# Optimization experiments

Hardware: AMD Instinct MI355X
Metric: run time of the kernel (lower is better)

The kernel has to match this reference:

```python
import jax, jax.numpy as jnp
import numpy as np

B, N, C, H = 2, 4096, 256, 4
DH = C // H  # 64
EPS = 1e-6
TEMPERATURE = 1.0


def setup_inputs() -> dict:
    key = jax.random.key(0)
    ks = jax.random.split(key, 12)
    s = 0.02
    return {
        "x": jax.random.normal(ks[0], (B, N, C), dtype=jnp.float32),
        "pos_embed": jax.random.normal(ks[1], (B, N, C), dtype=jnp.float32),
        # per-head Q/K/V linear weights stacked over heads (torch Linear(dim, dim_head))
        "Wq": jax.random.normal(ks[2], (H, C, DH), dtype=jnp.float32) * s,
        "bq": jax.random.normal(ks[3], (H, DH), dtype=jnp.float32) * s,
        "Wk": jax.random.normal(ks[4], (H, C, DH), dtype=jnp.float32) * s,
        "bk": jax.random.normal(ks[5], (H, DH), dtype=jnp.float32) * s,
        "Wv": jax.random.normal(ks[6], (H, C, DH), dtype=jnp.float32) * s,
        "bv": jax.random.normal(ks[7], (H, DH), dtype=jnp.float32) * s,
        "Wo": jax.random.normal(ks[8], (C, C), dtype=jnp.float32) * s,
        "bo": jax.random.normal(ks[9], (C,), dtype=jnp.float32) * s,
        "ln_g": jnp.ones((C,), dtype=jnp.float32),
        "ln_b": jnp.zeros((C,), dtype=jnp.float32),
    }


def reference(x, pos_embed, Wq, bq, Wk, bk, Wv, bv, Wo, bo, ln_g, ln_b):
    dk = TEMPERATURE * jnp.sqrt(jnp.float32(DH))
    # pre-norm: x + pos_embed -> dropout(p=0, identity) -> LayerNorm(eps=1e-6)
    h = x + pos_embed
    mu = jnp.mean(h, axis=-1, keepdims=True)
    var = jnp.mean(jnp.square(h - mu), axis=-1, keepdims=True)
    h = (h - mu) * jax.lax.rsqrt(var + EPS) * ln_g + ln_b  # [B,N,C]
    # all heads at once (original loops over heads with separate small Linears)
    q = jnp.einsum("bnc,hcd->bhnd", h, Wq) + bq[None, :, None, :]
    k = jnp.einsum("bnc,hcd->bhnd", h, Wk) + bk[None, :, None, :]
    v = jnp.einsum("bnc,hcd->bhnd", h, Wv) + bv[None, :, None, :]
    scores = jnp.einsum("bhid,bhjd->bhij", q, k) / dk  # [B,H,N,N]
    # NOTE: original uses F.softmax(dot_prod, dim=1) on [B,N,N] -> normalize over
    # the QUERY axis i, not the key axis j. Replicated faithfully here (axis=2).
    attn = jax.nn.softmax(scores, axis=2)
    o = jnp.einsum("bhij,bhjd->bhid", attn, v)  # [B,H,N,DH]
    o = jnp.transpose(o, (0, 2, 1, 3)).reshape(B, N, C)  # concat heads on channel
    return o @ Wo + bo
```

## Files before the change

kernel.cpp:

```cpp
#include <hip/hip_runtime.h>
#include <math.h>

#define B_ 2
#define N_ 4096
#define C_ 256
#define H_ 4
#define DH_ 64
#define EPS_ 1e-6f
#define SCALE_Q_ 0.18033688011112042f

typedef short bf16x8 __attribute__((ext_vector_type(8)));
typedef float f32x4 __attribute__((ext_vector_type(4)));
typedef int i32x4 __attribute__((ext_vector_type(4)));

#define MFMA32(a, b, c) __builtin_amdgcn_mfma_f32_16x16x32_bf16(a, b, c, 0, 0, 0)
#define FAST_EXP2(x) __builtin_amdgcn_exp2f(x)

__device__ __forceinline__ unsigned short f2bf(float x) {
  unsigned int u = __float_as_uint(x);
  return (unsigned short)((u + 0x7FFFu + ((u >> 16) & 1u)) >> 16);
}
__device__ __forceinline__ float bf2f(unsigned short u) {
  return __uint_as_float(((unsigned int)u) << 16);
}
__device__ __forceinline__ int pack2bf(float lo, float hi) {
  return (int)__builtin_amdgcn_perm(__float_as_uint(hi) + 0x8000u,
                                    __float_as_uint(lo) + 0x8000u, 0x07060302u);
}

__global__ __launch_bounds__(256) void ln_kernel(
    const float* __restrict__ x, const float* __restrict__ pos,
    const float* __restrict__ g, const float* __restrict__ beta,
    unsigned short* __restrict__ h16) {
  const int row = blockIdx.x;
  const int t = threadIdx.x;
  const int w = t >> 6;
  float val = x[row * C_ + t] + pos[row * C_ + t];
  __shared__ float sm[8];
  float s = val;
  s += __shfl_xor(s, 1);  s += __shfl_xor(s, 2);  s += __shfl_xor(s, 4);
  s += __shfl_xor(s, 8);  s += __shfl_xor(s, 16); s += __shfl_xor(s, 32);
  if ((t & 63) == 0) sm[w] = s;
  __syncthreads();
  const float mu = (sm[0] + sm[1] + sm[2] + sm[3]) * (1.0f / C_);
  const float d = val - mu;
  float v = d * d;
  v += __shfl_xor(v, 1);  v += __shfl_xor(v, 2);  v += __shfl_xor(v, 4);
  v += __shfl_xor(v, 8);  v += __shfl_xor(v, 16); v += __shfl_xor(v, 32);
  if ((t & 63) == 0) sm[4 + w] = v;
  __syncthreads();
  const float var = (sm[4] + sm[5] + sm[6] + sm[7]) * (1.0f / C_);
  h16[row * C_ + t] = f2bf(d * rsqrtf(var + EPS_) * g[t] + beta[t]);
}

__global__ __launch_bounds__(256) void wconv_kernel(
    const float* __restrict__ Wq, const float* __restrict__ Wk,
    const float* __restrict__ Wv, const float* __restrict__ Wo,
    unsigned short* __restrict__ W3T, unsigned short* __restrict__ WoT) {
  const int base = blockIdx.x * 2048;
#pragma unroll
  for (int p = 0; p < 8; p++) {
    const int idx = base + p * 256 + threadIdx.x;
    if (idx < 196608) {
      const int m = idx >> 14;
      const int rem = idx & 16383;
      const int c = rem >> 6, d = rem & 63;
      const int h = m / 3, kind = m - h * 3;
      const float* W = kind == 0 ? Wq : kind == 1 ? Wk : Wv;
      float v = W[h * 16384 + rem];
      if (kind == 0) v *= SCALE_Q_;
      W3T[(h * 192 + kind * 64 + d) * 256 + c] = f2bf(v);
    } else {
      const int widx = idx - 196608;
      const int k = widx >> 8, n = widx & 255;
      WoT[n * 256 + k] = f2bf(Wo[widx]);
    }
  }
}

__global__ __launch_bounds__(256) void qkv_kernel(
    const unsigned short* __restrict__ h16, const unsigned short* __restrict__ W3T,
    const float* __restrict__ bq, const float* __restrict__ bk,
    const float* __restrict__ bv,
    unsigned short* __restrict__ q16, unsigned short* __restrict__ k16,
    unsigned short* __restrict__ vT16) {
  const int rt = blockIdx.x;
  const int hh = blockIdx.y;
  const int t = threadIdx.x;
  const int w = t >> 6, lane = t & 63, c = lane & 15, quad = lane >> 4;
  __shared__ unsigned short Hs[128 * 64];
  __shared__ unsigned short Bs[192 * 64];
  const int row0 = rt * 128;

  f32x4 acc[2][12];
#pragma unroll
  for (int mi = 0; mi < 2; mi++)
#pragma unroll
    for (int nt = 0; nt < 12; nt++) acc[mi][nt] = (f32x4){0.f, 0.f, 0.f, 0.f};

  for (int kt = 0; kt < C_; kt += 64) {
    __syncthreads();
#pragma unroll
    for (int p = 0; p < 4; p++) {
      const int e = t + p * 256;
      const int row = e >> 3, ch = e & 7;
      *(bf16x8*)&Hs[row * 64 + ((ch ^ (row & 7)) * 8)] =
          *(const bf16x8*)&h16[(size_t)(row0 + row) * C_ + kt + ch * 8];
    }
#pragma unroll
    for (int p = 0; p < 6; p++) {
      const int e = t + p * 256;
      const int row = e >> 3, ch = e & 7;
      *(bf16x8*)&Bs[row * 64 + ((ch ^ (row & 7)) * 8)] =
          *(const bf16x8*)&W3T[(size_t)(hh * 192 + row) * C_ + kt + ch * 8];
    }
    __syncthreads();
#pragma unroll
    for (int kh = 0; kh < 2; kh++) {
      bf16x8 a[2];
#pragma unroll
      for (int mi = 0; mi < 2; mi++) {
        const int i = w * 32 + mi * 16 + c;
        a[mi] = *(const bf16x8*)&Hs[i * 64 + (((kh * 4 + quad) ^ (i & 7)) * 8)];
      }
#pragma unroll
      for (int nt = 0; nt < 12; nt++) {
        const int n = nt * 16 + c;
        bf16x8 b = *(const bf16x8*)&Bs[n * 64 + (((kh * 4 + quad) ^ (n & 7)) * 8)];
        acc[0][nt] = MFMA32(a[0], b, acc[0][nt]);
        acc[1][nt] = MFMA32(a[1], b, acc[1][nt]);
      }
    }
  }
#pragma unroll
  for (int nt = 0; nt < 12; nt++) {
    const int kind = nt >> 2;
    const int col = (nt & 3) * 16 + c;
    const float bias = kind == 0 ? bq[hh * 64 + col] * SCALE_Q_
                     : kind == 1 ? bk[hh * 64 + col] : bv[hh * 64 + col];
#pragma unroll
    for (int mi = 0; mi < 2; mi++) {
#pragma unroll
      for (int r = 0; r < 4; r++) {
        const int gr = row0 + w * 32 + mi * 16 + quad * 4 + r;
        const int b = gr >> 12, n = gr & (N_ - 1);
        const size_t bh = (size_t)(b * H_ + hh);
        const unsigned short val = f2bf(acc[mi][nt][r] + bias);
        if (kind == 0)      q16[(bh * N_ + n) * DH_ + col] = val;
        else if (kind == 1) k16[(bh * N_ + n) * DH_ + col] = val;
        else                vT16[(bh * DH_ + col) * N_ + n] = val;
      }
    }
  }
}

__global__ __launch_bounds__(256, 2) void colstats_kernel(
    const unsigned short* __restrict__ q16, const unsigned short* __restrict__ k16,
    unsigned short* __restrict__ vT16) {
  const int blk = blockIdx.x;
  const int bh = blk & 7;
  const int j0 = (blk >> 3) * 64;
  const int t = threadIdx.x;
  const int w = t >> 6, lane = t & 63, c = lane & 15, quad = lane >> 4;
  __shared__ unsigned short Qs[64 * 64];
  __shared__ float Lp[4][64];
  __shared__ float ilv[64];

  bf16x8 ka[4][2];
#pragma unroll
  for (int jb = 0; jb < 4; jb++) {
    const size_t kb = ((size_t)bh * N_ + j0 + jb * 16 + c) * DH_;
    ka[jb][0] = *(const bf16x8*)&k16[kb + quad * 8];
    ka[jb][1] = *(const bf16x8*)&k16[kb + 32 + quad * 8];
  }

  bf16x8 pre[2];
  auto loadQ = [&](int i0) {
#pragma unroll
    for (int p = 0; p < 2; p++) {
      const int e = t + p * 256;
      const int row = e >> 3, ch = e & 7;
      pre[p] = *(const bf16x8*)&q16[((size_t)bh * N_ + i0 + row) * DH_ + ch * 8];
    }
  };
  loadQ(0);

  f32x4 lsum[4];
#pragma unroll
  for (int jb = 0; jb < 4; jb++) lsum[jb] = (f32x4){0.f, 0.f, 0.f, 0.f};

  for (int i0 = 0; i0 < N_; i0 += 64) {
    __syncthreads();
#pragma unroll
    for (int p = 0; p < 2; p++) {
      const int e = t + p * 256;
      const int row = e >> 3, ch = e & 7;
      *(bf16x8*)&Qs[row * 64 + ((ch ^ (row & 7)) * 8)] = pre[p];
    }
    __syncthreads();
    if (i0 + 64 < N_) loadQ(i0 + 64);
    const int ir = w * 16 + c;
    bf16x8 qf0 = *(const bf16x8*)&Qs[ir * 64 + ((quad ^ (c & 7)) * 8)];
    bf16x8 qf1 = *(const bf16x8*)&Qs[ir * 64 + (((4 + quad) ^ (c & 7)) * 8)];
#pragma unroll
    for (int jb = 0; jb < 4; jb++) {
      f32x4 s = {0.f, 0.f, 0.f, 0.f};
      s = MFMA32(ka[jb][0], qf0, s);
      s = MFMA32(ka[jb][1], qf1, s);
#pragma unroll
      for (int r = 0; r < 4; r++) lsum[jb][r] += FAST_EXP2(s[r]);
    }
  }
#pragma unroll
  for (int jb = 0; jb < 4; jb++) {
#pragma unroll
    for (int r = 0; r < 4; r++) {
      float s = lsum[jb][r];
      s += __shfl_xor(s, 1); s += __shfl_xor(s, 2);
      s += __shfl_xor(s, 4); s += __shfl_xor(s, 8);
      if (c == 0) Lp[w][jb * 16 + quad * 4 + r] = s;
    }
  }
  __syncthreads();
  if (t < 64) ilv[t] = 1.0f / (Lp[0][t] + Lp[1][t] + Lp[2][t] + Lp[3][t]);
  __syncthreads();
#pragma unroll
  for (int p = 0; p < 2; p++) {
    const int e = t + p * 256;
    const int d = e >> 3, ch = e & 7;
    const size_t addr = ((size_t)bh * DH_ + d) * N_ + j0 + ch * 8;
    bf16x8 v = *(const bf16x8*)&vT16[addr];
#pragma unroll
    for (int jj = 0; jj < 8; jj++)
      v[jj] = (short)f2bf(bf2f((unsigned short)v[jj]) * ilv[ch * 8 + jj]);
    *(bf16x8*)&vT16[addr] = v;
  }
}

__global__ __launch_bounds__(256, 2) void attnout_kernel(
    const unsigned short* __restrict__ q16, const unsigned short* __restrict__ k16,
    const unsigned short* __restrict__ vT16, unsigned short* __restrict__ ob16) {
  const int blk = blockIdx.x;
  const int bh = blk & 7;
  const int bb = bh >> 2, hh = bh & 3;
  const int i0 = (blk >> 3) * 64;
  const int t = threadIdx.x;
  const int w = t >> 6, lane = t & 63, c = lane & 15, quad = lane >> 4;

  __shared__ unsigned short Ks[128 * 64];
  __shared__ unsigned short Vs[64 * 128];
  __shared__ float Rbuf[4096];

  bf16x8 qa[4][2];
#pragma unroll
  for (int ib = 0; ib < 4; ib++) {
    const size_t qb = ((size_t)bh * N_ + i0 + ib * 16 + c) * DH_;
    qa[ib][0] = *(const bf16x8*)&q16[qb + quad * 8];
    qa[ib][1] = *(const bf16x8*)&q16[qb + 32 + quad * 8];
  }

  bf16x8 kpre[4], vpre[4];
  auto loadKV = [&](int jt) {
#pragma unroll
    for (int p = 0; p < 4; p++) {
      const int e = t + p * 256;
      kpre[p] = *(const bf16x8*)&k16[((size_t)bh * N_ + jt + (e >> 3)) * DH_ + (e & 7) * 8];
      vpre[p] = *(const bf16x8*)&vT16[((size_t)bh * DH_ + (e >> 4)) * N_ + jt + (e & 15) * 8];
    }
  };
  loadKV(0);

  f32x4 of[4][4];
#pragma unroll
  for (int ib = 0; ib < 4; ib++)
#pragma unroll
    for (int dt = 0; dt < 4; dt++) of[ib][dt] = (f32x4){0.f, 0.f, 0.f, 0.f};

  const int jw = w * 32;
  for (int jt = 0; jt < N_; jt += 128) {
    __syncthreads();
#pragma unroll
    for (int p = 0; p < 4; p++) {
      const int e = t + p * 256;
      { const int row = e >> 3, ch = e & 7;
        *(bf16x8*)&Ks[row * 64 + ((ch ^ ((row >> 2) & 7)) * 8)] = kpre[p]; }
      { const int row = e >> 4, ch = e & 15;
        *(bf16x8*)&Vs[row * 128 + ((ch ^ (row & 15)) * 8)] = vpre[p]; }
    }
    __syncthreads();
    if (jt + 128 < N_) loadKV(jt + 128);

    bf16x8 kf[2][2];
#pragma unroll
    for (int s = 0; s < 2; s++) {
      const int jr = jw + ((c >> 2) * 8) + s * 4 + (c & 3);
      const int swz = (jr >> 2) & 7;
      kf[s][0] = *(const bf16x8*)&Ks[jr * 64 + ((quad ^ swz) * 8)];
      kf[s][1] = *(const bf16x8*)&Ks[jr * 64 + (((4 + quad) ^ swz) * 8)];
    }
    bf16x8 vf[4];
#pragma unroll
    for (int dt = 0; dt < 4; dt++) {
      const int d = dt * 16 + c;
      vf[dt] = *(const bf16x8*)&Vs[d * 128 + (((w * 4 + quad) ^ (d & 15)) * 8)];
    }

#pragma unroll
    for (int ib = 0; ib < 4; ib++) {
      f32x4 s0 = {0.f, 0.f, 0.f, 0.f}, s1 = {0.f, 0.f, 0.f, 0.f};
      s0 = MFMA32(kf[0][0], qa[ib][0], s0);
      s0 = MFMA32(kf[0][1], qa[ib][1], s0);
      s1 = MFMA32(kf[1][0], qa[ib][0], s1);
      s1 = MFMA32(kf[1][1], qa[ib][1], s1);
      i32x4 pi;
      pi[0] = pack2bf(FAST_EXP2(s0[0]), FAST_EXP2(s0[1]));
      pi[1] = pack2bf(FAST_EXP2(s0[2]), FAST_EXP2(s0[3]));
      pi[2] = pack2bf(FAST_EXP2(s1[0]), FAST_EXP2(s1[1]));
      pi[3] = pack2bf(FAST_EXP2(s1[2]), FAST_EXP2(s1[3]));
      bf16x8 pf = *(bf16x8*)&pi;
#pragma unroll
      for (int dt = 0; dt < 4; dt++)
        of[ib][dt] = MFMA32(pf, vf[dt], of[ib][dt]);
    }
  }

  for (int p = 1; p < 4; ++p) {
    __syncthreads();
    if (w == p) {
#pragma unroll
      for (int ib = 0; ib < 4; ib++)
#pragma unroll
        for (int dt = 0; dt < 4; dt++)
          *(f32x4*)&Rbuf[lane * 64 + (((ib * 4 + dt) ^ (lane & 15)) * 4)] = of[ib][dt];
    }
    __syncthreads();
    if (w == 0) {
#pragma unroll
      for (int ib = 0; ib < 4; ib++)
#pragma unroll
        for (int dt = 0; dt < 4; dt++)
          of[ib][dt] += *(const f32x4*)&Rbuf[lane * 64 + (((ib * 4 + dt) ^ (lane & 15)) * 4)];
    }
  }
  if (w == 0) {
#pragma unroll
    for (int ib = 0; ib < 4; ib++)
#pragma unroll
      for (int dt = 0; dt < 4; dt++)
#pragma unroll
        for (int r = 0; r < 4; r++)
          ob16[((size_t)bb * N_ + i0 + ib * 16 + quad * 4 + r) * C_ + hh * DH_ + dt * 16 + c] =
              f2bf(of[ib][dt][r]);
  }
}

__global__ __launch_bounds__(256) void outproj_kernel(
    const unsigned short* __restrict__ ob16, const unsigned short* __restrict__ WoT,
    const float* __restrict__ bo, float* __restrict__ out) {
  const int rt = blockIdx.x;
  const int t = threadIdx.x;
  const int w = t >> 6, lane = t & 63, c = lane & 15, quad = lane >> 4;
  __shared__ unsigned short As[32 * 64];
  __shared__ unsigned short Bs[256 * 64];

  f32x4 acc[2][4];
#pragma unroll
  for (int mt = 0; mt < 2; mt++)
#pragma unroll
    for (int nt = 0; nt < 4; nt++) acc[mt][nt] = (f32x4){0.f, 0.f, 0.f, 0.f};

  for (int kt = 0; kt < C_; kt += 64) {
    __syncthreads();
    {
      const int row = t >> 3, ch = t & 7;
      *(bf16x8*)&As[row * 64 + ((ch ^ (row & 7)) * 8)] =
          *(const bf16x8*)&ob16[((size_t)rt * 32 + row) * C_ + kt + ch * 8];
    }
#pragma unroll
    for (int p = 0; p < 8; p++) {
      const int e = t + p * 256;
      const int row = e >> 3, ch = e & 7;
      *(bf16x8*)&Bs[row * 64 + ((ch ^ (row & 7)) * 8)] =
          *(const bf16x8*)&WoT[(size_t)row * C_ + kt + ch * 8];
    }
    __syncthreads();
#pragma unroll
    for (int kh = 0; kh < 2; kh++) {
      bf16x8 a[2];
#pragma unroll
      for (int mt = 0; mt < 2; mt++) {
        const int i = mt * 16 + c;
        a[mt] = *(const bf16x8*)&As[i * 64 + (((kh * 4 + quad) ^ (i & 7)) * 8)];
      }
#pragma unroll
      for (int nt = 0; nt < 4; nt++) {
        const int n = w * 64 + nt * 16 + c;
        bf16x8 b = *(const bf16x8*)&Bs[n * 64 + (((kh * 4 + quad) ^ (n & 7)) * 8)];
        acc[0][nt] = MFMA32(a[0], b, acc[0][nt]);
        acc[1][nt] = MFMA32(a[1], b, acc[1][nt]);
      }
    }
  }
#pragma unroll
  for (int mt = 0; mt < 2; mt++)
#pragma unroll
    for (int nt = 0; nt < 4; nt++) {
      const int col = w * 64 + nt * 16 + c;
      const float bias = bo[col];
#pragma unroll
      for (int r = 0; r < 4; r++)
        out[((size_t)rt * 32 + mt * 16 + quad * 4 + r) * C_ + col] = acc[mt][nt][r] + bias;
    }
}

extern "C" void kernel_launch(void* const* d_in, const int* in_sizes, int n_in,
                              void* d_out, int out_size, void* d_ws, size_t ws_size,
                              hipStream_t stream) {
  const float* x    = (const float*)d_in[0];
  const float* pos  = (const float*)d_in[1];
  const float* Wq   = (const float*)d_in[2];
  const float* bq   = (const float*)d_in[3];
  const float* Wk   = (const float*)d_in[4];
  const float* bk   = (const float*)d_in[5];
  const float* Wv   = (const float*)d_in[6];
  const float* bv   = (const float*)d_in[7];
  const float* Wo   = (const float*)d_in[8];
  const float* bo   = (const float*)d_in[9];
  const float* ln_g = (const float*)d_in[10];
  const float* ln_b = (const float*)d_in[11];
  float* out = (float*)d_out;

  const size_t SZ = (size_t)B_ * N_ * C_;
  unsigned short* h16  = (unsigned short*)d_ws;
  unsigned short* q16  = h16 + SZ;
  unsigned short* k16  = q16 + SZ;
  unsigned short* vT16 = k16 + SZ;
  unsigned short* ob16 = vT16 + SZ;
  unsigned short* W3T  = ob16 + SZ;
  unsigned short* WoT  = W3T + (size_t)H_ * 192 * 256;

  ln_kernel<<<B_ * N_, 256, 0, stream>>>(x, pos, ln_g, ln_b, h16);
  wconv_kernel<<<128, 256, 0, stream>>>(Wq, Wk, Wv, Wo, W3T, WoT);
  qkv_kernel<<<dim3(64, H_), 256, 0, stream>>>(h16, W3T, bq, bk, bv, q16, k16, vT16);
  colstats_kernel<<<512, 256, 0, stream>>>(q16, k16, vT16);
  attnout_kernel<<<512, 256, 0, stream>>>(q16, k16, vT16, ob16);
  outproj_kernel<<<256, 256, 0, stream>>>(ob16, WoT, bo, out);
}
```

Measured before the change: 195.5 us.

## Use 512-thread blocks for attention kernels and halve QKV row tiles

Doubles the thread count per block in the column-stats and attention-output kernels to eight waves. Each block now covers twice the key/query span per iteration and shares one LDS buffer between K/V staging and a tree-style cross-wave reduction. The QKV projection tile shrinks from 128 to 64 rows, which doubles its grid to put more blocks on the GPU. The aim is better occupancy and fewer loop iterations and syncs, at the cost of higher LDS use (64KB per block) and more reduction steps at the end of attention.

```diff
diff --git a/kernel.cpp b/kernel.cpp
--- a/kernel.cpp
+++ b/kernel.cpp
@@ -88,20 +88,18 @@
   const int hh = blockIdx.y;
   const int t = threadIdx.x;
   const int w = t >> 6, lane = t & 63, c = lane & 15, quad = lane >> 4;
-  __shared__ unsigned short Hs[128 * 64];
+  __shared__ unsigned short Hs[64 * 64];
   __shared__ unsigned short Bs[192 * 64];
-  const int row0 = rt * 128;
-
-  f32x4 acc[2][12];
-#pragma unroll
-  for (int mi = 0; mi < 2; mi++)
-#pragma unroll
-    for (int nt = 0; nt < 12; nt++) acc[mi][nt] = (f32x4){0.f, 0.f, 0.f, 0.f};
+  const int row0 = rt * 64;
+
+  f32x4 acc[12];
+#pragma unroll
+  for (int nt = 0; nt < 12; nt++) acc[nt] = (f32x4){0.f, 0.f, 0.f, 0.f};
 
   for (int kt = 0; kt < C_; kt += 64) {
     __syncthreads();
 #pragma unroll
-    for (int p = 0; p < 4; p++) {
+    for (int p = 0; p < 2; p++) {
       const int e = t + p * 256;
       const int row = e >> 3, ch = e & 7;
       *(bf16x8*)&Hs[row * 64 + ((ch ^ (row & 7)) * 8)] =
@@ -117,18 +115,13 @@
     __syncthreads();
 #pragma unroll
     for (int kh = 0; kh < 2; kh++) {
-      bf16x8 a[2];
-#pragma unroll
-      for (int mi = 0; mi < 2; mi++) {
-        const int i = w * 32 + mi * 16 + c;
-        a[mi] = *(const bf16x8*)&Hs[i * 64 + (((kh * 4 + quad) ^ (i & 7)) * 8)];
-      }
+      const int i = w * 16 + c;
+      bf16x8 a = *(const bf16x8*)&Hs[i * 64 + (((kh * 4 + quad) ^ (i & 7)) * 8)];
 #pragma unroll
       for (int nt = 0; nt < 12; nt++) {
         const int n = nt * 16 + c;
         bf16x8 b = *(const bf16x8*)&Bs[n * 64 + (((kh * 4 + quad) ^ (n & 7)) * 8)];
-        acc[0][nt] = MFMA32(a[0], b, acc[0][nt]);
-        acc[1][nt] = MFMA32(a[1], b, acc[1][nt]);
+        acc[nt] = MFMA32(a, b, acc[nt]);
       }
     }
   }
@@ -139,22 +132,19 @@
     const float bias = kind == 0 ? bq[hh * 64 + col] * SCALE_Q_
                      : kind == 1 ? bk[hh * 64 + col] : bv[hh * 64 + col];
 #pragma unroll
-    for (int mi = 0; mi < 2; mi++) {
-#pragma unroll
-      for (int r = 0; r < 4; r++) {
-        const int gr = row0 + w * 32 + mi * 16 + quad * 4 + r;
-        const int b = gr >> 12, n = gr & (N_ - 1);
-        const size_t bh = (size_t)(b * H_ + hh);
-        const unsigned short val = f2bf(acc[mi][nt][r] + bias);
-        if (kind == 0)      q16[(bh * N_ + n) * DH_ + col] = val;
-        else if (kind == 1) k16[(bh * N_ + n) * DH_ + col] = val;
-        else                vT16[(bh * DH_ + col) * N_ + n] = val;
-      }
-    }
-  }
-}
-
-__global__ __launch_bounds__(256, 2) void colstats_kernel(
+    for (int r = 0; r < 4; r++) {
+      const int gr = row0 + w * 16 + quad * 4 + r;
+      const int b = gr >> 12, n = gr & (N_ - 1);
+      const size_t bh = (size_t)(b * H_ + hh);
+      const unsigned short val = f2bf(acc[nt][r] + bias);
+      if (kind == 0)      q16[(bh * N_ + n) * DH_ + col] = val;
+      else if (kind == 1) k16[(bh * N_ + n) * DH_ + col] = val;
+      else                vT16[(bh * DH_ + col) * N_ + n] = val;
+    }
+  }
+}
+
+__global__ __launch_bounds__(512, 4) void colstats_kernel(
     const unsigned short* __restrict__ q16, const unsigned short* __restrict__ k16,
     unsigned short* __restrict__ vT16) {
   const int blk = blockIdx.x;
@@ -162,8 +152,8 @@
   const int j0 = (blk >> 3) * 64;
   const int t = threadIdx.x;
   const int w = t >> 6, lane = t & 63, c = lane & 15, quad = lane >> 4;
-  __shared__ unsigned short Qs[64 * 64];
-  __shared__ float Lp[4][64];
+  __shared__ unsigned short Qs[128 * 64];
+  __shared__ float Lp[8][64];
   __shared__ float ilv[64];
 
   bf16x8 ka[4][2];
@@ -178,7 +168,7 @@
   auto loadQ = [&](int i0) {
 #pragma unroll
     for (int p = 0; p < 2; p++) {
-      const int e = t + p * 256;
+      const int e = t + p * 512;
       const int row = e >> 3, ch = e & 7;
       pre[p] = *(const bf16x8*)&q16[((size_t)bh * N_ + i0 + row) * DH_ + ch * 8];
     }
@@ -189,16 +179,16 @@
 #pragma unroll
   for (int jb = 0; jb < 4; jb++) lsum[jb] = (f32x4){0.f, 0.f, 0.f, 0.f};
 
-  for (int i0 = 0; i0 < N_; i0 += 64) {
+  for (int i0 = 0; i0 < N_; i0 += 128) {
     __syncthreads();
 #pragma unroll
     for (int p = 0; p < 2; p++) {
-      const int e = t + p * 256;
+      const int e = t + p * 512;
       const int row = e >> 3, ch = e & 7;
       *(bf16x8*)&Qs[row * 64 + ((ch ^ (row & 7)) * 8)] = pre[p];
     }
     __syncthreads();
-    if (i0 + 64 < N_) loadQ(i0 + 64);
+    if (i0 + 128 < N_) loadQ(i0 + 128);
     const int ir = w * 16 + c;
     bf16x8 qf0 = *(const bf16x8*)&Qs[ir * 64 + ((quad ^ (c & 7)) * 8)];
     bf16x8 qf1 = *(const bf16x8*)&Qs[ir * 64 + (((4 + quad) ^ (c & 7)) * 8)];
@@ -222,12 +212,15 @@
     }
   }
   __syncthreads();
-  if (t < 64) ilv[t] = 1.0f / (Lp[0][t] + Lp[1][t] + Lp[2][t] + Lp[3][t]);
+  if (t < 64) {
+    float l = 0.f;
+#pragma unroll
+    for (int ww = 0; ww < 8; ww++) l += Lp[ww][t];
+    ilv[t] = 1.0f / l;
+  }
   __syncthreads();
-#pragma unroll
-  for (int p = 0; p < 2; p++) {
-    const int e = t + p * 256;
-    const int d = e >> 3, ch = e & 7;
+  {
+    const int d = t >> 3, ch = t & 7;
     const size_t addr = ((size_t)bh * DH_ + d) * N_ + j0 + ch * 8;
     bf16x8 v = *(const bf16x8*)&vT16[addr];
 #pragma unroll
@@ -237,7 +230,7 @@
   }
 }
 
-__global__ __launch_bounds__(256, 2) void attnout_kernel(
+__global__ __launch_bounds__(512, 4) void attnout_kernel(
     const unsigned short* __restrict__ q16, const unsigned short* __restrict__ k16,
     const unsigned short* __restrict__ vT16, unsigned short* __restrict__ ob16) {
   const int blk = blockIdx.x;
@@ -247,9 +240,10 @@
   const int t = threadIdx.x;
   const int w = t >> 6, lane = t & 63, c = lane & 15, quad = lane >> 4;
 
-  __shared__ unsigned short Ks[128 * 64];
-  __shared__ unsigned short Vs[64 * 128];
-  __shared__ float Rbuf[4096];
+  __shared__ char smem[65536];
+  unsigned short* Ks = (unsigned short*)smem;
+  unsigned short* Vs = (unsigned short*)smem + 256 * 64;
+  float* Rf = (float*)smem;
 
   bf16x8 qa[4][2];
 #pragma unroll
@@ -263,9 +257,9 @@
   auto loadKV = [&](int jt) {
 #pragma unroll
     for (int p = 0; p < 4; p++) {
-      const int e = t + p * 256;
+      const int e = t + p * 512;
       kpre[p] = *(const bf16x8*)&k16[((size_t)bh * N_ + jt + (e >> 3)) * DH_ + (e & 7) * 8];
-      vpre[p] = *(const bf16x8*)&vT16[((size_t)bh * DH_ + (e >> 4)) * N_ + jt + (e & 15) * 8];
+      vpre[p] = *(const bf16x8*)&vT16[((size_t)bh * DH_ + (e >> 5)) * N_ + jt + (e & 31) * 8];
     }
   };
   loadKV(0);
@@ -277,18 +271,18 @@
     for (int dt = 0; dt < 4; dt++) of[ib][dt] = (f32x4){0.f, 0.f, 0.f, 0.f};
 
   const int jw = w * 32;
-  for (int jt = 0; jt < N_; jt += 128) {
+  for (int jt = 0; jt < N_; jt += 256) {
     __syncthreads();
 #pragma unroll
     for (int p = 0; p < 4; p++) {
-      const int e = t + p * 256;
+      const int e = t + p * 512;
       { const int row = e >> 3, ch = e & 7;
         *(bf16x8*)&Ks[row * 64 + ((ch ^ ((row >> 2) & 7)) * 8)] = kpre[p]; }
-      { const int row = e >> 4, ch = e & 15;
-        *(bf16x8*)&Vs[row * 128 + ((ch ^ (row & 15)) * 8)] = vpre[p]; }
-    }
-    __syncthreads();
-    if (jt + 128 < N_) loadKV(jt + 128);
+      { const int d = e >> 5, ch = e & 31;
+        *(bf16x8*)&Vs[d * 256 + ((ch ^ (d & 31)) * 8)] = vpre[p]; }
+    }
+    __syncthreads();
+    if (jt + 256 < N_) loadKV(jt + 256);
 
     bf16x8 kf[2][2];
 #pragma unroll
@@ -302,7 +296,7 @@
 #pragma unroll
     for (int dt = 0; dt < 4; dt++) {
       const int d = dt * 16 + c;
-      vf[dt] = *(const bf16x8*)&Vs[d * 128 + (((w * 4 + quad) ^ (d & 15)) * 8)];
+      vf[dt] = *(const bf16x8*)&Vs[d * 256 + (((w * 4 + quad) ^ (d & 31)) * 8)];
     }
 
 #pragma unroll
@@ -324,22 +318,24 @@
     }
   }
 
-  for (int p = 1; p < 4; ++p) {
-    __syncthreads();
-    if (w == p) {
+  for (int half = 4; half >= 1; half >>= 1) {
+    __syncthreads();
+    if (w >= half && w < 2 * half) {
+      float* dst = Rf + (w - half) * 4096;
 #pragma unroll
       for (int ib = 0; ib < 4; ib++)
 #pragma unroll
         for (int dt = 0; dt < 4; dt++)
-          *(f32x4*)&Rbuf[lane * 64 + (((ib * 4 + dt) ^ (lane & 15)) * 4)] = of[ib][dt];
-    }
-    __syncthreads();
-    if (w == 0) {
+          *(f32x4*)&dst[lane * 64 + (((ib * 4 + dt) ^ (lane & 15)) * 4)] = of[ib][dt];
+    }
+    __syncthreads();
+    if (w < half) {
+      const float* src = Rf + w * 4096;
 #pragma unroll
       for (int ib = 0; ib < 4; ib++)
 #pragma unroll
         for (int dt = 0; dt < 4; dt++)
-          of[ib][dt] += *(const f32x4*)&Rbuf[lane * 64 + (((ib * 4 + dt) ^ (lane & 15)) * 4)];
+          of[ib][dt] += *(const f32x4*)&src[lane * 64 + (((ib * 4 + dt) ^ (lane & 15)) * 4)];
     }
   }
   if (w == 0) {
@@ -441,8 +437,8 @@
 
   ln_kernel<<<B_ * N_, 256, 0, stream>>>(x, pos, ln_g, ln_b, h16);
   wconv_kernel<<<128, 256, 0, stream>>>(Wq, Wk, Wv, Wo, W3T, WoT);
-  qkv_kernel<<<dim3(64, H_), 256, 0, stream>>>(h16, W3T, bq, bk, bv, q16, k16, vT16);
-  colstats_kernel<<<512, 256, 0, stream>>>(q16, k16, vT16);
-  attnout_kernel<<<512, 256, 0, stream>>>(q16, k16, vT16, ob16);
+  qkv_kernel<<<dim3(128, H_), 256, 0, stream>>>(h16, W3T, bq, bk, bv, q16, k16, vT16);
+  colstats_kernel<<<512, 512, 0, stream>>>(q16, k16, vT16);
+  attnout_kernel<<<512, 512, 0, stream>>>(q16, k16, vT16, ob16);
   outproj_kernel<<<256, 256, 0, stream>>>(ob16, WoT, bo, out);
 }
```

Result: slower. 780.8 us (+299.4%).

## Split attnout work across 8 waves with a 2x4 query/key wave grid

Applied to the files above, without the earlier changes.

Doubles the attnout block to 512 threads, arranged as 2 query-row groups by 4 key-column groups, so each wave holds half as many output accumulators and Q fragments. This cuts registers per wave so more waves can be resident, and it replaces the serial 4-step cross-wave reduction with a two-level tree that shares one aliased 32KB shared buffer. Each block now issues fewer loads per thread for the K/V tile. The cost is more waves contending for the same LDS tile and more barriers per iteration.

```diff
diff --git a/kernel.cpp b/kernel.cpp
--- a/kernel.cpp
+++ b/kernel.cpp
@@ -237,7 +237,7 @@
   }
 }
 
-__global__ __launch_bounds__(256, 2) void attnout_kernel(
+__global__ __launch_bounds__(512, 4) void attnout_kernel(
     const unsigned short* __restrict__ q16, const unsigned short* __restrict__ k16,
     const unsigned short* __restrict__ vT16, unsigned short* __restrict__ ob16) {
   const int blk = blockIdx.x;
@@ -246,46 +246,48 @@
   const int i0 = (blk >> 3) * 64;
   const int t = threadIdx.x;
   const int w = t >> 6, lane = t & 63, c = lane & 15, quad = lane >> 4;
-
-  __shared__ unsigned short Ks[128 * 64];
-  __shared__ unsigned short Vs[64 * 128];
-  __shared__ float Rbuf[4096];
-
-  bf16x8 qa[4][2];
-#pragma unroll
-  for (int ib = 0; ib < 4; ib++) {
-    const size_t qb = ((size_t)bh * N_ + i0 + ib * 16 + c) * DH_;
+  const int iw = w >> 2;
+  const int jw = w & 3;
+
+  __shared__ __align__(16) char smem[32768];
+  unsigned short* Ks = (unsigned short*)smem;
+  unsigned short* Vs = (unsigned short*)smem + 128 * 64;
+  float* Rf = (float*)smem;
+
+  bf16x8 qa[2][2];
+#pragma unroll
+  for (int ib = 0; ib < 2; ib++) {
+    const size_t qb = ((size_t)bh * N_ + i0 + iw * 32 + ib * 16 + c) * DH_;
     qa[ib][0] = *(const bf16x8*)&q16[qb + quad * 8];
     qa[ib][1] = *(const bf16x8*)&q16[qb + 32 + quad * 8];
   }
 
-  bf16x8 kpre[4], vpre[4];
+  bf16x8 kpre[2], vpre[2];
   auto loadKV = [&](int jt) {
 #pragma unroll
-    for (int p = 0; p < 4; p++) {
-      const int e = t + p * 256;
+    for (int p = 0; p < 2; p++) {
+      const int e = t + p * 512;
       kpre[p] = *(const bf16x8*)&k16[((size_t)bh * N_ + jt + (e >> 3)) * DH_ + (e & 7) * 8];
       vpre[p] = *(const bf16x8*)&vT16[((size_t)bh * DH_ + (e >> 4)) * N_ + jt + (e & 15) * 8];
     }
   };
   loadKV(0);
 
-  f32x4 of[4][4];
-#pragma unroll
-  for (int ib = 0; ib < 4; ib++)
+  f32x4 of[2][4];
+#pragma unroll
+  for (int ib = 0; ib < 2; ib++)
 #pragma unroll
     for (int dt = 0; dt < 4; dt++) of[ib][dt] = (f32x4){0.f, 0.f, 0.f, 0.f};
 
-  const int jw = w * 32;
   for (int jt = 0; jt < N_; jt += 128) {
     __syncthreads();
 #pragma unroll
-    for (int p = 0; p < 4; p++) {
-      const int e = t + p * 256;
+    for (int p = 0; p < 2; p++) {
+      const int e = t + p * 512;
       { const int row = e >> 3, ch = e & 7;
         *(bf16x8*)&Ks[row * 64 + ((ch ^ ((row >> 2) & 7)) * 8)] = kpre[p]; }
-      { const int row = e >> 4, ch = e & 15;
-        *(bf16x8*)&Vs[row * 128 + ((ch ^ (row & 15)) * 8)] = vpre[p]; }
+      { const int d = e >> 4, ch = e & 15;
+        *(bf16x8*)&Vs[d * 128 + ((ch ^ (d & 15)) * 8)] = vpre[p]; }
     }
     __syncthreads();
     if (jt + 128 < N_) loadKV(jt + 128);
@@ -293,7 +295,7 @@
     bf16x8 kf[2][2];
 #pragma unroll
     for (int s = 0; s < 2; s++) {
-      const int jr = jw + ((c >> 2) * 8) + s * 4 + (c & 3);
+      const int jr = jw * 32 + ((c >> 2) * 8) + s * 4 + (c & 3);
       const int swz = (jr >> 2) & 7;
       kf[s][0] = *(const bf16x8*)&Ks[jr * 64 + ((quad ^ swz) * 8)];
       kf[s][1] = *(const bf16x8*)&Ks[jr * 64 + (((4 + quad) ^ swz) * 8)];
@@ -302,11 +304,11 @@
 #pragma unroll
     for (int dt = 0; dt < 4; dt++) {
       const int d = dt * 16 + c;
-      vf[dt] = *(const bf16x8*)&Vs[d * 128 + (((w * 4 + quad) ^ (d & 15)) * 8)];
-    }
-
-#pragma unroll
-    for (int ib = 0; ib < 4; ib++) {
+      vf[dt] = *(const bf16x8*)&Vs[d * 128 + (((jw * 4 + quad) ^ (d & 15)) * 8)];
+    }
+
+#pragma unroll
+    for (int ib = 0; ib < 2; ib++) {
       f32x4 s0 = {0.f, 0.f, 0.f, 0.f}, s1 = {0.f, 0.f, 0.f, 0.f};
       s0 = MFMA32(kf[0][0], qa[ib][0], s0);
       s0 = MFMA32(kf[0][1], qa[ib][1], s0);
@@ -324,33 +326,46 @@
     }
   }
 
-  for (int p = 1; p < 4; ++p) {
-    __syncthreads();
-    if (w == p) {
-#pragma unroll
-      for (int ib = 0; ib < 4; ib++)
-#pragma unroll
-        for (int dt = 0; dt < 4; dt++)
-          *(f32x4*)&Rbuf[lane * 64 + (((ib * 4 + dt) ^ (lane & 15)) * 4)] = of[ib][dt];
-    }
-    __syncthreads();
-    if (w == 0) {
-#pragma unroll
-      for (int ib = 0; ib < 4; ib++)
-#pragma unroll
-        for (int dt = 0; dt < 4; dt++)
-          of[ib][dt] += *(const f32x4*)&Rbuf[lane * 64 + (((ib * 4 + dt) ^ (lane & 15)) * 4)];
-    }
-  }
-  if (w == 0) {
-#pragma unroll
-    for (int ib = 0; ib < 4; ib++)
+  __syncthreads();
+  if (jw >= 2) {
+    float* dst = Rf + (iw * 2 + (jw - 2)) * 2048;
+#pragma unroll
+    for (int ib = 0; ib < 2; ib++)
 #pragma unroll
       for (int dt = 0; dt < 4; dt++)
+        *(f32x4*)&dst[lane * 32 + (((ib * 4 + dt) ^ (lane & 7)) * 4)] = of[ib][dt];
+  }
+  __syncthreads();
+  if (jw < 2) {
+    const float* src = Rf + (iw * 2 + jw) * 2048;
+#pragma unroll
+    for (int ib = 0; ib < 2; ib++)
+#pragma unroll
+      for (int dt = 0; dt < 4; dt++)
+        of[ib][dt] += *(const f32x4*)&src[lane * 32 + (((ib * 4 + dt) ^ (lane & 7)) * 4)];
+  }
+  __syncthreads();
+  if (jw == 1) {
+    float* dst = Rf + iw * 2048;
+#pragma unroll
+    for (int ib = 0; ib < 2; ib++)
+#pragma unroll
+      for (int dt = 0; dt < 4; dt++)
+        *(f32x4*)&dst[lane * 32 + (((ib * 4 + dt) ^ (lane & 7)) * 4)] = of[ib][dt];
+  }
+  __syncthreads();
+  if (jw == 0) {
+    const float* src = Rf + iw * 2048;
+#pragma unroll
+    for (int ib = 0; ib < 2; ib++)
+#pragma unroll
+      for (int dt = 0; dt < 4; dt++) {
+        of[ib][dt] += *(const f32x4*)&src[lane * 32 + (((ib * 4 + dt) ^ (lane & 7)) * 4)];
 #pragma unroll
         for (int r = 0; r < 4; r++)
-          ob16[((size_t)bb * N_ + i0 + ib * 16 + quad * 4 + r) * C_ + hh * DH_ + dt * 16 + c] =
-              f2bf(of[ib][dt][r]);
+          ob16[((size_t)bb * N_ + i0 + iw * 32 + ib * 16 + quad * 4 + r) * C_ +
+               hh * DH_ + dt * 16 + c] = f2bf(of[ib][dt][r]);
+      }
   }
 }
 
@@ -443,6 +458,6 @@
   wconv_kernel<<<128, 256, 0, stream>>>(Wq, Wk, Wv, Wo, W3T, WoT);
   qkv_kernel<<<dim3(64, H_), 256, 0, stream>>>(h16, W3T, bq, bk, bv, q16, k16, vT16);
   colstats_kernel<<<512, 256, 0, stream>>>(q16, k16, vT16);
-  attnout_kernel<<<512, 256, 0, stream>>>(q16, k16, vT16, ob16);
+  attnout_kernel<<<512, 512, 0, stream>>>(q16, k16, vT16, ob16);
   outproj_kernel<<<256, 256, 0, stream>>>(ob16, WoT, bo, out);
 }
```

After: 190.5 us. 2.6% less time.
